# Kernel tuning notes

Measured on AMD Instinct MI355X. Metric: run time of the kernel, lower is better.

## Reference

```python
import jax, jax.numpy as jnp
import numpy as np

NUM_HEADS = 16
NUM_KV_HEADS = 4
HEAD_DIM = 128
EPS = 1e-6


def _rotate_half(x):
    x1, x2 = jnp.split(x, 2, axis=-1)
    return jnp.concatenate((-x2, x1), axis=-1)


def _rms_norm(x, w):
    var = jnp.mean(x * x, axis=-1, keepdims=True)
    return x * jax.lax.rsqrt(var + EPS) * w


def setup_inputs() -> dict:
    key = jax.random.key(0)
    ks = jax.random.split(key, 6)
    B, S, H = 2, 2048, 2048
    hidden_states = jax.random.normal(ks[0], (B, S, H), dtype=jnp.float32)
    # real RoPE tables (HF-style: freqs tiled twice along last dim)
    inv_freq = 1.0 / (10000.0 ** (np.arange(0, HEAD_DIM, 2, dtype=np.float32) / HEAD_DIM))
    pos = np.arange(S, dtype=np.float32)
    ang = np.concatenate([pos[:, None] * inv_freq[None, :]] * 2, axis=-1)  # [S, head_dim]
    cos = jnp.broadcast_to(jnp.cos(ang)[None], (B, S, HEAD_DIM)).astype(jnp.float32)
    sin = jnp.broadcast_to(jnp.sin(ang)[None], (B, S, HEAD_DIM)).astype(jnp.float32)
    sc = 0.02
    Wq = jax.random.normal(ks[1], (NUM_HEADS * HEAD_DIM, H), dtype=jnp.float32) * sc
    Wk = jax.random.normal(ks[2], (NUM_KV_HEADS * HEAD_DIM, H), dtype=jnp.float32) * sc
    Wv = jax.random.normal(ks[3], (NUM_KV_HEADS * HEAD_DIM, H), dtype=jnp.float32) * sc
    Wo = jax.random.normal(ks[4], (H, NUM_HEADS * HEAD_DIM), dtype=jnp.float32) * sc
    q_norm_w = jnp.ones((HEAD_DIM,), dtype=jnp.float32)
    k_norm_w = jnp.ones((HEAD_DIM,), dtype=jnp.float32)
    return {"hidden_states": hidden_states, "cos": cos, "sin": sin,
            "Wq": Wq, "Wk": Wk, "Wv": Wv, "Wo": Wo,
            "q_norm_w": q_norm_w, "k_norm_w": k_norm_w}


def reference(hidden_states, cos, sin, Wq, Wk, Wv, Wo, q_norm_w, k_norm_w):
    B, S, H = hidden_states.shape
    groups = NUM_HEADS // NUM_KV_HEADS
    # projections (Linear: x @ W^T), then [B, h, S, d]
    q = (hidden_states @ Wq.T).reshape(B, S, NUM_HEADS, HEAD_DIM).transpose(0, 2, 1, 3)
    k = (hidden_states @ Wk.T).reshape(B, S, NUM_KV_HEADS, HEAD_DIM).transpose(0, 2, 1, 3)
    v = (hidden_states @ Wv.T).reshape(B, S, NUM_KV_HEADS, HEAD_DIM).transpose(0, 2, 1, 3)
    # per-head RMSNorm
    q = _rms_norm(q, q_norm_w)
    k = _rms_norm(k, k_norm_w)
    # RoPE, cos/sin broadcast over heads (unsqueeze_dim=1)
    c = cos[:, None, :, :]
    s = sin[:, None, :, :]
    q = q * c + _rotate_half(q) * s
    k = k * c + _rotate_half(k) * s
    # GQA: expand kv heads
    k = jnp.repeat(k, groups, axis=1)
    v = jnp.repeat(v, groups, axis=1)
    scale = 1.0 / jnp.sqrt(jnp.float32(HEAD_DIM))
    scores = jnp.einsum('bhqd,bhkd->bhqk', q, k) * scale
    attn = jax.nn.softmax(scores, axis=-1)
    out = jnp.einsum('bhqk,bhkd->bhqd', attn, v)
    out = out.transpose(0, 2, 1, 3).reshape(B, S, NUM_HEADS * HEAD_DIM)
    return out @ Wo.T
```

## Files before the change

kernel.cpp:

```cpp
#include <hip/hip_runtime.h>
#include <hip/hip_bf16.h>
#include <stdint.h>

typedef __attribute__((ext_vector_type(8))) short short8;
typedef __attribute__((ext_vector_type(4))) float floatx4;
typedef __attribute__((ext_vector_type(16))) float floatx16;

#define MFMA16(a, b, c) __builtin_amdgcn_mfma_f32_16x16x32_bf16(a, b, c, 0, 0, 0)
#define MFMA32(a, b, c) __builtin_amdgcn_mfma_f32_32x32x16_bf16(a, b, c, 0, 0, 0)

static __device__ __forceinline__ void gload_lds16(const __hip_bfloat16* g, __hip_bfloat16* l) {
  __builtin_amdgcn_global_load_lds(
      (const __attribute__((address_space(1))) void*)g,
      (__attribute__((address_space(3))) void*)l,
      16, 0, 0);
}

__global__ __launch_bounds__(256)
void f2bf_all(const float* __restrict__ h, const float* __restrict__ wq,
              const float* __restrict__ wk, const float* __restrict__ wv,
              const float* __restrict__ wo, __hip_bfloat16* __restrict__ hb,
              __hip_bfloat16* __restrict__ wqkv, __hip_bfloat16* __restrict__ wob) {
  const int blk = blockIdx.x;
  const float* src;
  __hip_bfloat16* dst;
  int off;
  if (blk < 8192)       { src = h;  dst = hb;                          off = blk; }
  else if (blk < 12288) { src = wq; dst = wqkv;                        off = blk - 8192; }
  else if (blk < 13312) { src = wk; dst = wqkv + (size_t)2048 * 2048;  off = blk - 12288; }
  else if (blk < 14336) { src = wv; dst = wqkv + (size_t)2560 * 2048;  off = blk - 13312; }
  else                  { src = wo; dst = wob;                         off = blk - 14336; }
  const int i = off * 1024 + threadIdx.x * 4;
  const float4 v = *(const float4*)(src + i);
  __hip_bfloat16 t[4] = {__float2bfloat16(v.x), __float2bfloat16(v.y),
                         __float2bfloat16(v.z), __float2bfloat16(v.w)};
  *(short4*)(dst + i) = *(const short4*)t;
}

template <typename OUT_T>
__global__ __launch_bounds__(256)
void gemm_bt(const __hip_bfloat16* __restrict__ A, const __hip_bfloat16* __restrict__ Bt,
             OUT_T* __restrict__ C, int M, int N, int K) {
  __shared__ __hip_bfloat16 As[2][128 * 32];
  __shared__ __hip_bfloat16 Bs[2][128 * 32];
  const int tid = threadIdx.x;
  const int wid = tid >> 6, lane = tid & 63;
  const int lg = lane >> 4, lr = lane & 15;
  const int wr = wid >> 1, wc = wid & 1;
  const int m0 = blockIdx.x * 128, n0 = blockIdx.y * 128;
  const int nk = K >> 5;

  floatx4 acc[4][4];
#pragma unroll
  for (int mi = 0; mi < 4; ++mi)
#pragma unroll
    for (int ni = 0; ni < 4; ++ni) acc[mi][ni] = (floatx4)(0.0f);

  auto stage = [&](int buf, int kt) {
    const int k0 = kt << 5;
#pragma unroll
    for (int i = 0; i < 2; ++i) {
      const int e = (i * 256 + tid) * 8;
      const int row = e >> 5, col = e & 31;
      gload_lds16(A + (size_t)(m0 + row) * K + k0 + col, &As[buf][e]);
    }
#pragma unroll
    for (int i = 0; i < 2; ++i) {
      const int e = (i * 256 + tid) * 8;
      const int row = e >> 5, col = e & 31;
      gload_lds16(Bt + (size_t)(n0 + row) * K + k0 + col, &Bs[buf][e]);
    }
  };

  stage(0, 0);
  __syncthreads();

  for (int kt = 0; kt < nk; ++kt) {
    const int cur = kt & 1;
    if (kt + 1 < nk) stage(cur ^ 1, kt + 1);
    short8 af[4], bfr[4];
#pragma unroll
    for (int mi = 0; mi < 4; ++mi)
      af[mi] = *(const short8*)&As[cur][(wr * 64 + mi * 16 + lr) * 32 + lg * 8];
#pragma unroll
    for (int ni = 0; ni < 4; ++ni)
      bfr[ni] = *(const short8*)&Bs[cur][(wc * 64 + ni * 16 + lr) * 32 + lg * 8];
#pragma unroll
    for (int mi = 0; mi < 4; ++mi)
#pragma unroll
      for (int ni = 0; ni < 4; ++ni) acc[mi][ni] = MFMA16(af[mi], bfr[ni], acc[mi][ni]);
    __syncthreads();
  }

#pragma unroll
  for (int mi = 0; mi < 4; ++mi)
#pragma unroll
    for (int ni = 0; ni < 4; ++ni) {
      const int row = m0 + wr * 64 + mi * 16 + lg * 4;
      const int col = n0 + wc * 64 + ni * 16 + lr;
#pragma unroll
      for (int r = 0; r < 4; ++r) {
        C[(size_t)(row + r) * N + col] = (OUT_T)acc[mi][ni][r];
      }
    }
}

__global__ __launch_bounds__(256)
void normrope(const __hip_bfloat16* __restrict__ qkv, const float* __restrict__ cosb,
              const float* __restrict__ sinb, const float* __restrict__ qw,
              const float* __restrict__ kw, __hip_bfloat16* __restrict__ Q,
              __hip_bfloat16* __restrict__ Kblk) {
  const int m = blockIdx.x;
  const int b = m >> 11, s = m & 2047;
  const int wid = threadIdx.x >> 6, lane = threadIdx.x & 63;
  const size_t qkvrow = (size_t)m * 3072;
  const float c1 = cosb[(size_t)m * 128 + lane], s1 = sinb[(size_t)m * 128 + lane];
  const float c2 = cosb[(size_t)m * 128 + lane + 64], s2 = sinb[(size_t)m * 128 + lane + 64];
  const float QS = 0.12753102497113446f;
  for (int h = wid * 5; h < wid * 5 + 5; ++h) {
    const float x1 = __bfloat162float(qkv[qkvrow + h * 128 + lane]);
    const float x2 = __bfloat162float(qkv[qkvrow + h * 128 + lane + 64]);
    float ss = x1 * x1 + x2 * x2;
    ss += __shfl_xor(ss, 1);  ss += __shfl_xor(ss, 2);  ss += __shfl_xor(ss, 4);
    ss += __shfl_xor(ss, 8);  ss += __shfl_xor(ss, 16); ss += __shfl_xor(ss, 32);
    const float rs = rsqrtf(ss * (1.0f / 128.0f) + 1e-6f);
    const float* w = (h < 16) ? qw : kw;
    const float n1 = x1 * rs * w[lane], n2 = x2 * rs * w[lane + 64];
    const float o1 = n1 * c1 - n2 * s1;
    const float o2 = n2 * c2 + n1 * s2;
    if (h < 16) {
      const size_t base = ((size_t)(b * 16 + h) * 2048 + s) * 128;
      Q[base + lane] = __float2bfloat16(o1 * QS);
      Q[base + lane + 64] = __float2bfloat16(o2 * QS);
    } else {
      const int z = b * 4 + (h - 16);
      const int t = s >> 6, kv = s & 63;
      const size_t base =
          (size_t)z * 262144 + t * 8192 + (lane >> 3) * 512 + kv * 8 + (lane & 7);
      Kblk[base] = __float2bfloat16(o1);
      Kblk[base + 4096] = __float2bfloat16(o2);
    }
  }
}

__global__ __launch_bounds__(256)
void vtrans2(const __hip_bfloat16* __restrict__ qkv, __hip_bfloat16* __restrict__ Vt2) {
  __shared__ short L[64 * 65];
  const int tid = threadIdx.x;
  const int t = blockIdx.x, d0 = blockIdx.y * 64, z = blockIdx.z;
  const int b = z >> 2, hkv = z & 3;
  const int s0 = t * 64;
#pragma unroll
  for (int i = 0; i < 2; ++i) {
    const int slot = i * 256 + tid;
    const int srow = slot >> 3, c8 = (slot & 7) * 8;
    const short8 v = *(const short8*)((const short*)qkv +
        (size_t)(b * 2048 + s0 + srow) * 3072 + 2560 + hkv * 128 + d0 + c8);
#pragma unroll
    for (int j = 0; j < 8; ++j) L[(c8 + j) * 65 + srow] = v[j];
  }
  __syncthreads();
  short* dst = (short*)Vt2 + (size_t)z * 262144 + t * 8192;
#pragma unroll
  for (int i = 0; i < 2; ++i) {
    const int slot = i * 256 + tid;
    const int drow = slot >> 3, sc8 = (slot & 7) * 8;
    short8 o;
#pragma unroll
    for (int j = 0; j < 8; ++j) {
      const int p = sc8 + j;
      const int pb = p & 31;
      const int phys = (p & ~31) | ((pb & 3) + ((pb >> 2) & 1) * 8 + ((pb >> 3) & 1) * 4 + (pb & 16));
      o[j] = L[drow * 65 + phys];
    }
    *(short8*)&dst[(sc8 >> 3) * 1024 + (d0 + drow) * 8] = o;
  }
}

__global__ __launch_bounds__(256, 2)
void fattn(const __hip_bfloat16* __restrict__ Qg, const __hip_bfloat16* __restrict__ Kb2,
           const __hip_bfloat16* __restrict__ Vt2, __hip_bfloat16* __restrict__ Og) {
  __shared__ short SMEM[40960];

  const int tid = threadIdx.x, wid = tid >> 6, lane = tid & 63;
  const int l31 = lane & 31, hi = lane >> 5;
  const int qt = blockIdx.x, bh = blockIdx.y;
  const int b = bh >> 4, h = bh & 15, hkv = h >> 2;
  const int z = b * 4 + hkv;
  const int q0w = qt * 128 + wid * 32;

  const __hip_bfloat16* Qrow = Qg + ((size_t)((b * 16 + h) * 2048 + q0w + l31)) * 128;
  short8 qf2[8];
#pragma unroll
  for (int ks = 0; ks < 8; ++ks) qf2[ks] = *(const short8*)(Qrow + ks * 16 + hi * 8);

  const short* Kbase = (const short*)Kb2 + (size_t)z * 262144;
  const short* Vbase = (const short*)Vt2 + (size_t)z * 262144;

  auto stageK = [&](int buf, int t) {
    const short* ks = Kbase + t * 8192 + wid * 2048 + lane * 8;
    short* kd = &SMEM[buf * 8192 + wid * 2048];
#pragma unroll
    for (int i = 0; i < 4; ++i)
      gload_lds16((const __hip_bfloat16*)(ks + i * 512), (__hip_bfloat16*)(kd + i * 512));
  };
  auto stageV = [&](int slot, int t) {
    const short* vs = Vbase + t * 8192 + wid * 2048 + lane * 8;
    short* vd = &SMEM[16384 + slot * 8192 + wid * 2048];
#pragma unroll
    for (int i = 0; i < 4; ++i)
      gload_lds16((const __hip_bfloat16*)(vs + i * 512), (__hip_bfloat16*)(vd + i * 512));
  };

  floatx16 oacc[4];
#pragma unroll
  for (int dblk = 0; dblk < 4; ++dblk) oacc[dblk] = (floatx16)(0.0f);
  floatx16 lacc = (floatx16)(0.0f);

  short8 ones;
#pragma unroll
  for (int j = 0; j < 8; ++j) ones[j] = (short)0x3F80;

  int pkA[2][8], pkB[2][8];

  auto doQK = [&](int kbuf, floatx16 (&st)[2]) {
    const short* Kt = &SMEM[kbuf * 8192];
    st[0] = (floatx16)(0.0f);
    st[1] = (floatx16)(0.0f);
    __builtin_amdgcn_s_setprio(1);
#pragma unroll
    for (int ks = 0; ks < 8; ++ks) {
      const short8 kf0 = *(const short8*)&Kt[(ks * 2 + hi) * 512 + l31 * 8];
      const short8 kf1 = *(const short8*)&Kt[(ks * 2 + hi) * 512 + 256 + l31 * 8];
      st[0] = MFMA32(kf0, qf2[ks], st[0]);
      st[1] = MFMA32(kf1, qf2[ks], st[1]);
    }
    __builtin_amdgcn_s_setprio(0);
  };
  auto doExp = [&](const floatx16 (&st)[2], int (&pk)[2][8]) {
#pragma unroll
    for (int kvblk = 0; kvblk < 2; ++kvblk)
#pragma unroll
      for (int m = 0; m < 8; ++m) {
        const float e0 = exp2f(st[kvblk][2 * m]);
        const float e1 = exp2f(st[kvblk][2 * m + 1]);
        asm("v_cvt_pk_bf16_f32 %0, %1, %2" : "=v"(pk[kvblk][m]) : "v"(e0), "v"(e1));
      }
  };
  auto doPV = [&](int vslot, const int (&pk)[2][8]) {
    const short* Vt = &SMEM[16384 + vslot * 8192];
#pragma unroll
    for (int kvblk = 0; kvblk < 2; ++kvblk) {
#pragma unroll
      for (int s = 0; s < 2; ++s) {
        union { int i[4]; short8 s8; } u;
        u.i[0] = pk[kvblk][4 * s + 0];
        u.i[1] = pk[kvblk][4 * s + 1];
        u.i[2] = pk[kvblk][4 * s + 2];
        u.i[3] = pk[kvblk][4 * s + 3];
        const short8 pB = u.s8;
        const int c = kvblk * 4 + s * 2 + hi;
        __builtin_amdgcn_s_setprio(1);
        lacc = MFMA32(ones, pB, lacc);
#pragma unroll
        for (int dblk = 0; dblk < 4; ++dblk) {
          const short8 vf = *(const short8*)&Vt[c * 1024 + dblk * 256 + l31 * 8];
          oacc[dblk] = MFMA32(vf, pB, oacc[dblk]);
        }
        __builtin_amdgcn_s_setprio(0);
      }
    }
  };

  int vs_stage = 2, vs_pv = 0;
  auto body = [&](int (&pkPrev)[2][8], int (&pkCur)[2][8], int u) {
    if (u + 1 < 32) {
      stageK((u + 1) & 1, u + 1);
      stageV(vs_stage, u + 1);
    }
    floatx16 st[2];
    doQK(u & 1, st);
    doPV(vs_pv, pkPrev);
    doExp(st, pkCur);
    vs_stage = (vs_stage == 2) ? 0 : vs_stage + 1;
    vs_pv = (vs_pv == 2) ? 0 : vs_pv + 1;
    asm volatile("s_waitcnt vmcnt(0)" ::: "memory");
    __builtin_amdgcn_s_barrier();
    __builtin_amdgcn_sched_barrier(0);
  };

  stageK(0, 0);
  stageV(0, 0);
  asm volatile("s_waitcnt vmcnt(0)" ::: "memory");
  __builtin_amdgcn_s_barrier();
  __builtin_amdgcn_sched_barrier(0);
  {
    stageK(1, 1);
    stageV(1, 1);
    floatx16 st[2];
    doQK(0, st);
    doExp(st, pkA);
    asm volatile("s_waitcnt vmcnt(0)" ::: "memory");
    __builtin_amdgcn_s_barrier();
    __builtin_amdgcn_sched_barrier(0);
  }

  for (int u = 1; u < 31; u += 2) {
    body(pkA, pkB, u);
    body(pkB, pkA, u + 1);
  }
  body(pkA, pkB, 31);
  doPV(vs_pv, pkB);

  asm volatile("s_waitcnt lgkmcnt(0)" ::: "memory");
  __builtin_amdgcn_s_barrier();

  const float inv = 1.0f / lacc[0];
  short* tw = &SMEM[wid * 4352];
#pragma unroll
  for (int dblk = 0; dblk < 4; ++dblk)
#pragma unroll
    for (int a = 0; a < 4; ++a) {
      __hip_bfloat16 o4[4];
#pragma unroll
      for (int r = 0; r < 4; ++r) o4[r] = __float2bfloat16(oacc[dblk][4 * a + r] * inv);
      *(short4*)&tw[l31 * 136 + dblk * 32 + a * 8 + hi * 4] = *(const short4*)o4;
    }
  __hip_bfloat16* orow =
      Og + ((size_t)(b * 2048 + q0w + (lane >> 1))) * 2048 + h * 128 + (lane & 1) * 64;
  const short* trow = &tw[(lane >> 1) * 136 + (lane & 1) * 64];
#pragma unroll
  for (int c = 0; c < 8; ++c) {
    *(short8*)(orow + c * 8) = *(const short8*)(trow + c * 8);
  }
}

extern "C" void kernel_launch(void* const* d_in, const int* in_sizes, int n_in,
                              void* d_out, int out_size, void* d_ws, size_t ws_size,
                              hipStream_t stream) {
  const float* hidden = (const float*)d_in[0];
  const float* cosb = (const float*)d_in[1];
  const float* sinb = (const float*)d_in[2];
  const float* Wq = (const float*)d_in[3];
  const float* Wk = (const float*)d_in[4];
  const float* Wv = (const float*)d_in[5];
  const float* Wo = (const float*)d_in[6];
  const float* qw = (const float*)d_in[7];
  const float* kw = (const float*)d_in[8];

  char* ws = (char*)d_ws;
  __hip_bfloat16* hidden_bf = (__hip_bfloat16*)ws; ws += (size_t)4096 * 2048 * 2;
  __hip_bfloat16* wqkv = (__hip_bfloat16*)ws;      ws += (size_t)3072 * 2048 * 2;
  __hip_bfloat16* wo_bf = (__hip_bfloat16*)ws;     ws += (size_t)2048 * 2048 * 2;
  __hip_bfloat16* qkv = (__hip_bfloat16*)ws;       ws += (size_t)4096 * 3072 * 2;
  __hip_bfloat16* Qb = (__hip_bfloat16*)ws;        ws += (size_t)2 * 16 * 2048 * 128 * 2;
  __hip_bfloat16* Kblk = (__hip_bfloat16*)ws;      ws += (size_t)2 * 4 * 2048 * 128 * 2;
  __hip_bfloat16* attn = (__hip_bfloat16*)ws;      ws += (size_t)4096 * 2048 * 2;
  __hip_bfloat16* Vt2 = wqkv;

  f2bf_all<<<18432, 256, 0, stream>>>(hidden, Wq, Wk, Wv, Wo, hidden_bf, wqkv, wo_bf);

  gemm_bt<__hip_bfloat16><<<dim3(32, 24), 256, 0, stream>>>(hidden_bf, wqkv, qkv, 4096, 3072, 2048);
  normrope<<<4096, 256, 0, stream>>>(qkv, cosb, sinb, qw, kw, Qb, Kblk);
  vtrans2<<<dim3(32, 2, 8), 256, 0, stream>>>(qkv, Vt2);
  fattn<<<dim3(16, 32), 256, 0, stream>>>(Qb, Kblk, Vt2, attn);
  gemm_bt<float><<<dim3(32, 16), 256, 0, stream>>>(attn, wo_bf, (float*)d_out, 4096, 2048, 2048);
}
```

Measured before the change: 229.6 us.

## Triple-buffer GEMM LDS with XOR swizzle and grouped block rasterization

Rewrites the bf16 GEMM main loop to use three LDS stages with explicit vmcnt waits, so two tiles of global-to-LDS loads stay in flight while computing. It also XOR-swizzles the 16-byte column groups in LDS to reduce bank conflicts on fragment reads. Workgroup IDs are remapped so neighbouring blocks share tiles in cache. The cost is 50% more LDS per block, which may lower occupancy, and the hand-written waitcnt and barrier logic can break if the compiler reorders memory operations.

```diff
diff --git a/kernel.cpp b/kernel.cpp
--- a/kernel.cpp
+++ b/kernel.cpp
@@ -41,14 +41,20 @@
 __global__ __launch_bounds__(256)
 void gemm_bt(const __hip_bfloat16* __restrict__ A, const __hip_bfloat16* __restrict__ Bt,
              OUT_T* __restrict__ C, int M, int N, int K) {
-  __shared__ __hip_bfloat16 As[2][128 * 32];
-  __shared__ __hip_bfloat16 Bs[2][128 * 32];
+  __shared__ short LDS[3 * 8192];
+
   const int tid = threadIdx.x;
   const int wid = tid >> 6, lane = tid & 63;
   const int lg = lane >> 4, lr = lane & 15;
   const int wr = wid >> 1, wc = wid & 1;
-  const int m0 = blockIdx.x * 128, n0 = blockIdx.y * 128;
+
+  const int nwg = gridDim.x * gridDim.y;
+  const int orig = blockIdx.y * gridDim.x + blockIdx.x;
+  const int swz = (orig & 7) * (nwg >> 3) + (orig >> 3);
+  const int m0 = (swz % gridDim.x) * 128, n0 = (swz / gridDim.x) * 128;
   const int nk = K >> 5;
+
+  const int axor = (lg ^ ((lr >> 1) & 3)) * 8;
 
   floatx4 acc[4][4];
 #pragma unroll
@@ -58,38 +64,60 @@
 
   auto stage = [&](int buf, int kt) {
     const int k0 = kt << 5;
+    short* dst = &LDS[buf * 8192];
 #pragma unroll
     for (int i = 0; i < 2; ++i) {
-      const int e = (i * 256 + tid) * 8;
-      const int row = e >> 5, col = e & 31;
-      gload_lds16(A + (size_t)(m0 + row) * K + k0 + col, &As[buf][e]);
+      const int c = i * 256 + tid;
+      const int row = c >> 2;
+      const int gp = (c & 3) ^ ((row >> 1) & 3);
+      gload_lds16(A + (size_t)(m0 + row) * K + k0 + gp * 8, (__hip_bfloat16*)(dst + c * 8));
     }
 #pragma unroll
     for (int i = 0; i < 2; ++i) {
-      const int e = (i * 256 + tid) * 8;
-      const int row = e >> 5, col = e & 31;
-      gload_lds16(Bt + (size_t)(n0 + row) * K + k0 + col, &Bs[buf][e]);
-    }
+      const int c = i * 256 + tid;
+      const int row = c >> 2;
+      const int gp = (c & 3) ^ ((row >> 1) & 3);
+      gload_lds16(Bt + (size_t)(n0 + row) * K + k0 + gp * 8,
+                  (__hip_bfloat16*)(dst + 4096 + c * 8));
+    }
+  };
+
+  auto compute = [&](int buf) {
+    const short* base = &LDS[buf * 8192];
+    short8 af[4], bfr[4];
+#pragma unroll
+    for (int mi = 0; mi < 4; ++mi) {
+      const int row = wr * 64 + mi * 16 + lr;
+      af[mi] = *(const short8*)&base[row * 32 + axor];
+    }
+#pragma unroll
+    for (int ni = 0; ni < 4; ++ni) {
+      const int row = wc * 64 + ni * 16 + lr;
+      bfr[ni] = *(const short8*)&base[4096 + row * 32 + axor];
+    }
+#pragma unroll
+    for (int mi = 0; mi < 4; ++mi)
+#pragma unroll
+      for (int ni = 0; ni < 4; ++ni) acc[mi][ni] = MFMA16(af[mi], bfr[ni], acc[mi][ni]);
   };
 
   stage(0, 0);
-  __syncthreads();
+  stage(1, 1);
+  asm volatile("s_waitcnt vmcnt(4)" ::: "memory");
+  __builtin_amdgcn_s_barrier();
+  __builtin_amdgcn_sched_barrier(0);
 
   for (int kt = 0; kt < nk; ++kt) {
-    const int cur = kt & 1;
-    if (kt + 1 < nk) stage(cur ^ 1, kt + 1);
-    short8 af[4], bfr[4];
-#pragma unroll
-    for (int mi = 0; mi < 4; ++mi)
-      af[mi] = *(const short8*)&As[cur][(wr * 64 + mi * 16 + lr) * 32 + lg * 8];
-#pragma unroll
-    for (int ni = 0; ni < 4; ++ni)
-      bfr[ni] = *(const short8*)&Bs[cur][(wc * 64 + ni * 16 + lr) * 32 + lg * 8];
-#pragma unroll
-    for (int mi = 0; mi < 4; ++mi)
-#pragma unroll
-      for (int ni = 0; ni < 4; ++ni) acc[mi][ni] = MFMA16(af[mi], bfr[ni], acc[mi][ni]);
-    __syncthreads();
+    if (kt + 2 < nk) {
+      stage((kt + 2) % 3, kt + 2);
+      compute(kt % 3);
+      asm volatile("s_waitcnt vmcnt(4)" ::: "memory");
+    } else {
+      compute(kt % 3);
+      asm volatile("s_waitcnt vmcnt(0)" ::: "memory");
+    }
+    __builtin_amdgcn_s_barrier();
+    __builtin_amdgcn_sched_barrier(0);
   }
 
 #pragma unroll
```

New measurement: 270.6 us. +17.9%, slower.
